# Optimization experiments

Hardware: AMD Instinct MI355X
Metric: run time of the kernel (lower is better)

Reference implementation:

```python
import jax, jax.numpy as jnp
import numpy as np

_DIMS = [15, 30, 60, 90, 120, 90, 60, 30, 15, 10, 5, 1]


def setup_inputs() -> dict:
    key = jax.random.key(0)
    keys = jax.random.split(key, 1 + 2 * 11)
    inp = {"x": jax.random.normal(keys[0], (524288, 15), dtype=jnp.float32)}
    for i in range(11):
        fan_in, fan_out = _DIMS[i], _DIMS[i + 1]
        bound = 1.0 / np.sqrt(fan_in)
        inp[f"W{i+1}"] = jax.random.uniform(keys[1 + 2 * i], (fan_out, fan_in), minval=-bound, maxval=bound, dtype=jnp.float32)
        inp[f"b{i+1}"] = jax.random.uniform(keys[2 + 2 * i], (fan_out,), minval=-bound, maxval=bound, dtype=jnp.float32)
    return inp


def reference(x, W1, b1, W2, b2, W3, b3, W4, b4, W5, b5, W6, b6, W7, b7, W8, b8, W9, b9, W10, b10, W11, b11):
    Ws = [W1, W2, W3, W4, W5, W6, W7, W8, W9, W10, W11]
    bs = [b1, b2, b3, b4, b5, b6, b7, b8, b9, b10, b11]
    h = x
    # 10 Linear+ReLU layers, funnel 15->30->60->90->120->90->60->30->15->10->5
    for W, b in zip(Ws[:-1], bs[:-1]):
        h = jax.nn.relu(h @ W.T + b)
    # final Linear 5->1 + sigmoid
    return jax.nn.sigmoid(h @ Ws[-1].T + bs[-1])
```

## Files before the change

### kernel.cpp

```cpp
#include <hip/hip_runtime.h>
#include <math.h>


using bf16x8 = __attribute__((ext_vector_type(8))) short;
using f32x4  = __attribute__((ext_vector_type(4))) float;
using u16x8  = __attribute__((ext_vector_type(8))) unsigned short;
using u32x2  = __attribute__((ext_vector_type(2))) unsigned;
typedef __bf16 bf16x2_t __attribute__((ext_vector_type(2)));

namespace {
constexpr int NL = 11;
constexpr int IN_[NL]   = {15, 30, 60, 90, 120, 90, 60, 30, 15, 10, 5};
constexpr int OUT_[NL]  = {30, 60, 90, 120, 90, 60, 30, 15, 10, 5, 1};
constexpr int KP_[NL]   = {32, 32, 64, 96, 128, 96, 64, 32, 32, 32, 32};
constexpr int NP_[NL]   = {32, 64, 96, 128, 96, 64, 32, 16, 16, 16, 16};
constexpr int WOFF_[NL] = {0, 1024, 3072, 9216, 21504, 33792, 39936, 41984, 42496, 43008, 43520};
constexpr int WTOT      = 44032;
constexpr int ACT_OFF   = WTOT;
constexpr int WAVES     = 16;
constexpr int THREADS   = WAVES * 64;
constexpr int ROWS_PER_WAVE  = 16;
constexpr int ROWS_PER_BLOCK = WAVES * ROWS_PER_WAVE;
constexpr int ARENA     = 2048;
constexpr int LDS_BYTES = (WTOT + WAVES * ARENA) * 2;
}

__device__ __forceinline__ unsigned short f2bf(float f) {
    unsigned u = __float_as_uint(f);
    u += 0x7fffu + ((u >> 16) & 1u);
    return (unsigned short)(u >> 16);
}

__device__ __forceinline__ unsigned pk2(float a, float b) {
#if __has_builtin(__builtin_amdgcn_cvt_pk_bf16_f32)
    return __builtin_bit_cast(unsigned, __builtin_amdgcn_cvt_pk_bf16_f32(a, b));
#else
    bf16x2_t c;
    c[0] = (__bf16)a;
    c[1] = (__bf16)b;
    return __builtin_bit_cast(unsigned, c);
#endif
}

template <int L>
__device__ __forceinline__ void stage_w(const float* __restrict__ W,
                                        const float* __restrict__ B,
                                        short* wlds, int tid) {
    constexpr int KP = KP_[L], NP = NP_[L], INl = IN_[L], OUTl = OUT_[L];
    constexpr int NKT = KP / 32;
    for (int idx = tid; idx < NP * KP; idx += THREADS) {
        const int f    = idx >> 9;
        const int t    = idx & 511;
        const int quad = t >> 7;
        const int colc = (t >> 3) & 15;
        const int j    = t & 7;
        const int mt   = f / NKT;
        const int kt   = f - mt * NKT;
        const int m    = mt * 16 + colc;
        const int k    = kt * 32 + quad * 8 + j;
        float v = 0.f;
        if (m < OUTl) {
            if (k < INl) v = W[m * INl + k];
            else if (k == INl) v = B[m];
            else if (k == INl + 1) {
                float hf = __builtin_bit_cast(float, (unsigned)f2bf(B[m]) << 16);
                v = B[m] - hf;
            }
        } else if (m == OUTl || m == OUTl + 1) {
            if (k == INl) v = 1.f;
        }
        wlds[WOFF_[L] + idx] = (short)f2bf(v);
    }
}

template <int L>
__device__ __forceinline__ void layer_fwd(const short* __restrict__ wlds,
                                          short* buf, int col, int quad) {
    constexpr int KP   = KP_[L];
    constexpr int NP   = NP_[L];
    constexpr int NKT  = KP / 32;
    constexpr int NMT  = NP / 16;
    constexpr int KPN  = KP_[L + 1];
    const short* wl = wlds + WOFF_[L];
    const int fo = quad * 128 + col * 8;

    f32x4 acc[NMT];
#pragma unroll
    for (int mt = 0; mt < NMT; ++mt)
        acc[mt] = f32x4{0.f, 0.f, 0.f, 0.f};

#pragma unroll
    for (int kt = 0; kt < NKT; ++kt) {
        bf16x8 b0 = *(const bf16x8*)(buf + kt * 512 + fo);
#pragma unroll
        for (int mt = 0; mt < NMT; ++mt) {
            bf16x8 af = *(const bf16x8*)(wl + (mt * NKT + kt) * 512 + fo);
            acc[mt] = __builtin_amdgcn_mfma_f32_16x16x32_bf16(af, b0, acc[mt], 0, 0, 0);
        }
    }
#pragma unroll
    for (int mt = 0; mt < NMT; ++mt) {
        const int wbase = (mt >> 1) * 512 + ((mt & 1) * 2 + (quad >> 1)) * 128 + col * 8 + (quad & 1) * 4;
        u32x2 o;
        o[0] = pk2(fmaxf(acc[mt][0], 0.f), fmaxf(acc[mt][1], 0.f));
        o[1] = pk2(fmaxf(acc[mt][2], 0.f), fmaxf(acc[mt][3], 0.f));
        *(u32x2*)(buf + wbase) = o;
    }
    if constexpr (NP < KPN) {
        if (quad < 2) {
            u16x8 z = {0, 0, 0, 0, 0, 0, 0, 0};
            if (quad == 0) z[0] = (unsigned short)0x3F80;
            *(u16x8*)(buf + (2 + quad) * 128 + col * 8) = z;
        }
    }
}

__device__ __forceinline__ void layer_one(bf16x8 af, short* buf, int col, int quad) {
    const int fo = quad * 128 + col * 8;
    bf16x8 b0 = *(const bf16x8*)(buf + fo);
    f32x4 a0 = f32x4{0.f, 0.f, 0.f, 0.f};
    a0 = __builtin_amdgcn_mfma_f32_16x16x32_bf16(af, b0, a0, 0, 0, 0);
    const int wbase = (quad >> 1) * 128 + col * 8 + (quad & 1) * 4;
    u32x2 o0;
    o0[0] = pk2(fmaxf(a0[0], 0.f), fmaxf(a0[1], 0.f));
    o0[1] = pk2(fmaxf(a0[2], 0.f), fmaxf(a0[3], 0.f));
    *(u32x2*)(buf + wbase) = o0;
    if (quad < 2) {
        u16x8 z = {0, 0, 0, 0, 0, 0, 0, 0};
        if (quad == 0) z[0] = (unsigned short)0x3F80;
        *(u16x8*)(buf + (2 + quad) * 128 + col * 8) = z;
    }
}

__device__ __forceinline__ float4 ld4(const float* p) {
    float4 t;
    __builtin_memcpy(&t, p, 16);
    return t;
}

__device__ __forceinline__ void fetch_x(const float* __restrict__ x, int row0,
                                        int col, int quad, float4& a0) {
    const float* r0 = x + (long)(row0 + col) * 15;
    if (quad < 3) {
        a0 = ld4(r0 + quad * 4);
    } else {
        float4 t0 = ld4(r0 + 11);
        a0 = make_float4(t0.y, t0.z, t0.w, 1.f);
    }
}

__device__ __forceinline__ void stage_x(short* buf, float4 a0, int col, int quad) {
    const int off = (quad >> 1) * 128 + col * 8 + (quad & 1) * 4;
    u32x2 o0;
    o0[0] = pk2(a0.x, a0.y); o0[1] = pk2(a0.z, a0.w);
    *(u32x2*)(buf + off) = o0;
    if (quad < 2) {
        u16x8 z = {0, 0, 0, 0, 0, 0, 0, 0};
        if (quad == 0) z[0] = (unsigned short)0x3F80;
        *(u16x8*)(buf + (2 + quad) * 128 + col * 8) = z;
    }
}

extern "C" __global__ void __launch_bounds__(THREADS, 4)
mlp_fused(const float* __restrict__ x,
          const float* __restrict__ W0,  const float* __restrict__ B0,
          const float* __restrict__ W1,  const float* __restrict__ B1,
          const float* __restrict__ W2,  const float* __restrict__ B2,
          const float* __restrict__ W3,  const float* __restrict__ B3,
          const float* __restrict__ W4,  const float* __restrict__ B4,
          const float* __restrict__ W5,  const float* __restrict__ B5,
          const float* __restrict__ W6,  const float* __restrict__ B6,
          const float* __restrict__ W7,  const float* __restrict__ B7,
          const float* __restrict__ W8,  const float* __restrict__ B8,
          const float* __restrict__ W9,  const float* __restrict__ B9,
          const float* __restrict__ W10, const float* __restrict__ B10,
          float* __restrict__ out, int nchunks) {
    extern __shared__ short smem[];
    short* wlds = smem;
    short* act  = smem + ACT_OFF;

    const int tid = threadIdx.x;

    stage_w<0>(W0, B0, wlds, tid);
    stage_w<1>(W1, B1, wlds, tid);
    stage_w<2>(W2, B2, wlds, tid);
    stage_w<3>(W3, B3, wlds, tid);
    stage_w<4>(W4, B4, wlds, tid);
    stage_w<5>(W5, B5, wlds, tid);
    stage_w<6>(W6, B6, wlds, tid);
    stage_w<7>(W7, B7, wlds, tid);
    stage_w<8>(W8, B8, wlds, tid);
    stage_w<9>(W9, B9, wlds, tid);
    stage_w<10>(W10, B10, wlds, tid);
    __syncthreads();

    const int wave = tid >> 6;
    const int lane = tid & 63;
    const int col  = lane & 15;
    const int quad = lane >> 4;
    short* buf = act + wave * ARENA;
    const int fo = quad * 128 + col * 8;

    const bf16x8 w7  = *(const bf16x8*)(wlds + WOFF_[7]  + fo);
    const bf16x8 w8  = *(const bf16x8*)(wlds + WOFF_[8]  + fo);
    const bf16x8 w9  = *(const bf16x8*)(wlds + WOFF_[9]  + fo);
    const bf16x8 w10 = *(const bf16x8*)(wlds + WOFF_[10] + fo);

    int chunk = blockIdx.x;
    float4 xa;
    if (chunk < nchunks)
        fetch_x(x, chunk * ROWS_PER_BLOCK + wave * ROWS_PER_WAVE, col, quad, xa);

    for (; chunk < nchunks; chunk += gridDim.x) {
        const int row0 = chunk * ROWS_PER_BLOCK + wave * ROWS_PER_WAVE;
        stage_x(buf, xa, col, quad);

        const int nxt = chunk + gridDim.x;
        if (nxt < nchunks)
            fetch_x(x, nxt * ROWS_PER_BLOCK + wave * ROWS_PER_WAVE, col, quad, xa);

        layer_fwd<0>(wlds, buf, col, quad);
        layer_fwd<1>(wlds, buf, col, quad);
        layer_fwd<2>(wlds, buf, col, quad);
        layer_fwd<3>(wlds, buf, col, quad);
        layer_fwd<4>(wlds, buf, col, quad);
        layer_fwd<5>(wlds, buf, col, quad);
        layer_fwd<6>(wlds, buf, col, quad);
        layer_one(w7, buf, col, quad);
        layer_one(w8, buf, col, quad);
        layer_one(w9, buf, col, quad);

        {
            bf16x8 b0 = *(const bf16x8*)(buf + fo);
            f32x4 a0 = f32x4{0.f, 0.f, 0.f, 0.f};
            a0 = __builtin_amdgcn_mfma_f32_16x16x32_bf16(w10, b0, a0, 0, 0, 0);
            if (quad == 0)
                out[row0 + col] = 1.f / (1.f + __expf(-a0[0]));
        }
    }
}

extern "C" void kernel_launch(void* const* d_in, const int* in_sizes, int n_in,
                              void* d_out, int out_size, void* d_ws, size_t ws_size,
                              hipStream_t stream) {
    (void)n_in; (void)d_ws; (void)ws_size; (void)out_size;
    const float* x = (const float*)d_in[0];
    const float* W[11];
    const float* B[11];
    for (int i = 0; i < 11; ++i) {
        W[i] = (const float*)d_in[1 + 2 * i];
        B[i] = (const float*)d_in[2 + 2 * i];
    }
    const int nrows   = in_sizes[0] / 15;
    const int nchunks = nrows / ROWS_PER_BLOCK;

    hipFuncSetAttribute((const void*)mlp_fused,
                        hipFuncAttributeMaxDynamicSharedMemorySize, LDS_BYTES);

    mlp_fused<<<dim3(256), dim3(THREADS), LDS_BYTES, stream>>>(
        x,
        W[0], B[0], W[1], B[1], W[2], B[2], W[3], B[3], W[4], B[4],
        W[5], B[5], W[6], B[6], W[7], B[7], W[8], B[8], W[9], B[9],
        W[10], B[10],
        (float*)d_out, nchunks);
}
```

Baseline: 182.9 us.

## Keep activations in registers using 32x32x16 MFMA and permlane32 swaps

Replaces the 16x16x32 MFMA chain, which staged every layer's activations through a per-wave LDS arena, with 32x32x16 MFMA tiles whose outputs are repacked into the next layer's B operand in registers via permlane32_swap. Each wave now handles 32 rows, and LDS holds only the weights. This removes the per-layer LDS write/read round trips and the fence-style dependencies they create. In exchange, register pressure rises (f32x16 accumulators plus two register activation buffers), the launch-bounds occupancy hint is dropped, and the small tail layers are padded to 32 outputs, which adds wasted MFMA work.

```diff
diff --git a/kernel.cpp b/kernel.cpp
--- a/kernel.cpp
+++ b/kernel.cpp
@@ -3,9 +3,9 @@
 
 
 using bf16x8 = __attribute__((ext_vector_type(8))) short;
-using f32x4  = __attribute__((ext_vector_type(4))) float;
-using u16x8  = __attribute__((ext_vector_type(8))) unsigned short;
-using u32x2  = __attribute__((ext_vector_type(2))) unsigned;
+using f32x16 = __attribute__((ext_vector_type(16))) float;
+using u32x2v = __attribute__((ext_vector_type(2))) unsigned;
+using u32x4  = __attribute__((ext_vector_type(4))) unsigned;
 typedef __bf16 bf16x2_t __attribute__((ext_vector_type(2)));
 
 namespace {
@@ -13,16 +13,15 @@
 constexpr int IN_[NL]   = {15, 30, 60, 90, 120, 90, 60, 30, 15, 10, 5};
 constexpr int OUT_[NL]  = {30, 60, 90, 120, 90, 60, 30, 15, 10, 5, 1};
 constexpr int KP_[NL]   = {32, 32, 64, 96, 128, 96, 64, 32, 32, 32, 32};
-constexpr int NP_[NL]   = {32, 64, 96, 128, 96, 64, 32, 16, 16, 16, 16};
-constexpr int WOFF_[NL] = {0, 1024, 3072, 9216, 21504, 33792, 39936, 41984, 42496, 43008, 43520};
-constexpr int WTOT      = 44032;
-constexpr int ACT_OFF   = WTOT;
+constexpr int NP_[NL]   = {32, 64, 96, 128, 96, 64, 32, 32, 32, 32, 32};
+constexpr int WOFF_[NL] = {0, 1024, 3072, 9216, 21504, 33792, 39936,
+                           41984, 43008, 44032, 45056};
+constexpr int WTOT      = 46080;
 constexpr int WAVES     = 16;
 constexpr int THREADS   = WAVES * 64;
-constexpr int ROWS_PER_WAVE  = 16;
+constexpr int ROWS_PER_WAVE  = 32;
 constexpr int ROWS_PER_BLOCK = WAVES * ROWS_PER_WAVE;
-constexpr int ARENA     = 2048;
-constexpr int LDS_BYTES = (WTOT + WAVES * ARENA) * 2;
+constexpr int LDS_BYTES = WTOT * 2;
 }
 
 __device__ __forceinline__ unsigned short f2bf(float f) {
@@ -42,22 +41,41 @@
 #endif
 }
 
+__device__ __forceinline__ u32x2v pls32(unsigned a, unsigned b) {
+#if __has_builtin(__builtin_amdgcn_permlane32_swap)
+    auto t = __builtin_amdgcn_permlane32_swap(a, b, false, false);
+    u32x2v r;
+    r[0] = t[0];
+    r[1] = t[1];
+    return r;
+#else
+    const int l = (int)(threadIdx.x & 63);
+    unsigned bl = (unsigned)__shfl((int)b, l & 31, 64);
+    unsigned ah = (unsigned)__shfl((int)a, l | 32, 64);
+    u32x2v r;
+    r[0] = (l < 32) ? a : bl;
+    r[1] = (l < 32) ? ah : b;
+    return r;
+#endif
+}
+
 template <int L>
 __device__ __forceinline__ void stage_w(const float* __restrict__ W,
                                         const float* __restrict__ B,
                                         short* wlds, int tid) {
     constexpr int KP = KP_[L], NP = NP_[L], INl = IN_[L], OUTl = OUT_[L];
-    constexpr int NKT = KP / 32;
+    constexpr int NKT = KP / 16;
     for (int idx = tid; idx < NP * KP; idx += THREADS) {
         const int f    = idx >> 9;
         const int t    = idx & 511;
-        const int quad = t >> 7;
-        const int colc = (t >> 3) & 15;
+        const int ln   = t >> 3;
         const int j    = t & 7;
+        const int mloc = ln & 31;
+        const int kh   = ln >> 5;
         const int mt   = f / NKT;
         const int kt   = f - mt * NKT;
-        const int m    = mt * 16 + colc;
-        const int k    = kt * 32 + quad * 8 + j;
+        const int m    = mt * 32 + mloc;
+        const int k    = kt * 16 + kh * 8 + j;
         float v = 0.f;
         if (m < OUTl) {
             if (k < INl) v = W[m * INl + k];
@@ -74,61 +92,32 @@
 }
 
 template <int L>
-__device__ __forceinline__ void layer_fwd(const short* __restrict__ wlds,
-                                          short* buf, int col, int quad) {
-    constexpr int KP   = KP_[L];
-    constexpr int NP   = NP_[L];
-    constexpr int NKT  = KP / 32;
-    constexpr int NMT  = NP / 16;
-    constexpr int KPN  = KP_[L + 1];
+__device__ __forceinline__ void layer(const short* __restrict__ wlds,
+                                      const u32x4* bin, u32x4* bout, int lofs) {
+    constexpr int NKT = KP_[L] / 16;
+    constexpr int NMT = NP_[L] / 32;
     const short* wl = wlds + WOFF_[L];
-    const int fo = quad * 128 + col * 8;
-
-    f32x4 acc[NMT];
-#pragma unroll
-    for (int mt = 0; mt < NMT; ++mt)
-        acc[mt] = f32x4{0.f, 0.f, 0.f, 0.f};
-
-#pragma unroll
-    for (int kt = 0; kt < NKT; ++kt) {
-        bf16x8 b0 = *(const bf16x8*)(buf + kt * 512 + fo);
-#pragma unroll
-        for (int mt = 0; mt < NMT; ++mt) {
-            bf16x8 af = *(const bf16x8*)(wl + (mt * NKT + kt) * 512 + fo);
-            acc[mt] = __builtin_amdgcn_mfma_f32_16x16x32_bf16(af, b0, acc[mt], 0, 0, 0);
+#pragma unroll
+    for (int mt = 0; mt < NMT; ++mt) {
+        f32x16 acc;
+#pragma unroll
+        for (int i = 0; i < 16; ++i) acc[i] = 0.f;
+#pragma unroll
+        for (int kt = 0; kt < NKT; ++kt) {
+            bf16x8 af = *(const bf16x8*)(wl + (mt * NKT + kt) * 512 + lofs);
+            acc = __builtin_amdgcn_mfma_f32_32x32x16_bf16(
+                af, __builtin_bit_cast(bf16x8, bin[kt]), acc, 0, 0, 0);
         }
-    }
-#pragma unroll
-    for (int mt = 0; mt < NMT; ++mt) {
-        const int wbase = (mt >> 1) * 512 + ((mt & 1) * 2 + (quad >> 1)) * 128 + col * 8 + (quad & 1) * 4;
-        u32x2 o;
-        o[0] = pk2(fmaxf(acc[mt][0], 0.f), fmaxf(acc[mt][1], 0.f));
-        o[1] = pk2(fmaxf(acc[mt][2], 0.f), fmaxf(acc[mt][3], 0.f));
-        *(u32x2*)(buf + wbase) = o;
-    }
-    if constexpr (NP < KPN) {
-        if (quad < 2) {
-            u16x8 z = {0, 0, 0, 0, 0, 0, 0, 0};
-            if (quad == 0) z[0] = (unsigned short)0x3F80;
-            *(u16x8*)(buf + (2 + quad) * 128 + col * 8) = z;
-        }
-    }
-}
-
-__device__ __forceinline__ void layer_one(bf16x8 af, short* buf, int col, int quad) {
-    const int fo = quad * 128 + col * 8;
-    bf16x8 b0 = *(const bf16x8*)(buf + fo);
-    f32x4 a0 = f32x4{0.f, 0.f, 0.f, 0.f};
-    a0 = __builtin_amdgcn_mfma_f32_16x16x32_bf16(af, b0, a0, 0, 0, 0);
-    const int wbase = (quad >> 1) * 128 + col * 8 + (quad & 1) * 4;
-    u32x2 o0;
-    o0[0] = pk2(fmaxf(a0[0], 0.f), fmaxf(a0[1], 0.f));
-    o0[1] = pk2(fmaxf(a0[2], 0.f), fmaxf(a0[3], 0.f));
-    *(u32x2*)(buf + wbase) = o0;
-    if (quad < 2) {
-        u16x8 z = {0, 0, 0, 0, 0, 0, 0, 0};
-        if (quad == 0) z[0] = (unsigned short)0x3F80;
-        *(u16x8*)(buf + (2 + quad) * 128 + col * 8) = z;
+        unsigned P[8];
+#pragma unroll
+        for (int i = 0; i < 8; ++i)
+            P[i] = pk2(fmaxf(acc[2 * i], 0.f), fmaxf(acc[2 * i + 1], 0.f));
+        u32x2v r02 = pls32(P[0], P[2]);
+        u32x2v r13 = pls32(P[1], P[3]);
+        u32x2v r46 = pls32(P[4], P[6]);
+        u32x2v r57 = pls32(P[5], P[7]);
+        bout[2 * mt]     = u32x4{r02[0], r13[0], r02[1], r13[1]};
+        bout[2 * mt + 1] = u32x4{r46[0], r57[0], r46[1], r57[1]};
     }
 }
 
@@ -138,30 +127,26 @@
     return t;
 }
 
-__device__ __forceinline__ void fetch_x(const float* __restrict__ x, int row0,
-                                        int col, int quad, float4& a0) {
-    const float* r0 = x + (long)(row0 + col) * 15;
-    if (quad < 3) {
-        a0 = ld4(r0 + quad * 4);
+__device__ __forceinline__ void fetch_x(const float* __restrict__ x, int row,
+                                        int h, float4& t0, float4& t1) {
+    const float* p = x + (long)row * 15;
+    if (h == 0) { t0 = ld4(p);     t1 = ld4(p + 4);  }
+    else        { t0 = ld4(p + 8); t1 = ld4(p + 11); }
+}
+
+__device__ __forceinline__ u32x4 pack_x(float4 t0, float4 t1, int h) {
+    u32x4 b;
+    if (h == 0) {
+        b[0] = pk2(t0.x, t0.y); b[1] = pk2(t0.z, t0.w);
+        b[2] = pk2(t1.x, t1.y); b[3] = pk2(t1.z, t1.w);
     } else {
-        float4 t0 = ld4(r0 + 11);
-        a0 = make_float4(t0.y, t0.z, t0.w, 1.f);
-    }
-}
-
-__device__ __forceinline__ void stage_x(short* buf, float4 a0, int col, int quad) {
-    const int off = (quad >> 1) * 128 + col * 8 + (quad & 1) * 4;
-    u32x2 o0;
-    o0[0] = pk2(a0.x, a0.y); o0[1] = pk2(a0.z, a0.w);
-    *(u32x2*)(buf + off) = o0;
-    if (quad < 2) {
-        u16x8 z = {0, 0, 0, 0, 0, 0, 0, 0};
-        if (quad == 0) z[0] = (unsigned short)0x3F80;
-        *(u16x8*)(buf + (2 + quad) * 128 + col * 8) = z;
-    }
-}
-
-extern "C" __global__ void __launch_bounds__(THREADS, 4)
+        b[0] = pk2(t0.x, t0.y); b[1] = pk2(t0.z, t0.w);
+        b[2] = pk2(t1.y, t1.z); b[3] = pk2(t1.w, 1.f);
+    }
+    return b;
+}
+
+extern "C" __global__ void __launch_bounds__(THREADS)
 mlp_fused(const float* __restrict__ x,
           const float* __restrict__ W0,  const float* __restrict__ B0,
           const float* __restrict__ W1,  const float* __restrict__ B1,
@@ -176,66 +161,66 @@
           const float* __restrict__ W10, const float* __restrict__ B10,
           float* __restrict__ out, int nchunks) {
     extern __shared__ short smem[];
-    short* wlds = smem;
-    short* act  = smem + ACT_OFF;
-
     const int tid = threadIdx.x;
 
-    stage_w<0>(W0, B0, wlds, tid);
-    stage_w<1>(W1, B1, wlds, tid);
-    stage_w<2>(W2, B2, wlds, tid);
-    stage_w<3>(W3, B3, wlds, tid);
-    stage_w<4>(W4, B4, wlds, tid);
-    stage_w<5>(W5, B5, wlds, tid);
-    stage_w<6>(W6, B6, wlds, tid);
-    stage_w<7>(W7, B7, wlds, tid);
-    stage_w<8>(W8, B8, wlds, tid);
-    stage_w<9>(W9, B9, wlds, tid);
-    stage_w<10>(W10, B10, wlds, tid);
+    stage_w<0>(W0, B0, smem, tid);
+    stage_w<1>(W1, B1, smem, tid);
+    stage_w<2>(W2, B2, smem, tid);
+    stage_w<3>(W3, B3, smem, tid);
+    stage_w<4>(W4, B4, smem, tid);
+    stage_w<5>(W5, B5, smem, tid);
+    stage_w<6>(W6, B6, smem, tid);
+    stage_w<7>(W7, B7, smem, tid);
+    stage_w<8>(W8, B8, smem, tid);
+    stage_w<9>(W9, B9, smem, tid);
+    stage_w<10>(W10, B10, smem, tid);
     __syncthreads();
 
     const int wave = tid >> 6;
     const int lane = tid & 63;
-    const int col  = lane & 15;
-    const int quad = lane >> 4;
-    short* buf = act + wave * ARENA;
-    const int fo = quad * 128 + col * 8;
-
-    const bf16x8 w7  = *(const bf16x8*)(wlds + WOFF_[7]  + fo);
-    const bf16x8 w8  = *(const bf16x8*)(wlds + WOFF_[8]  + fo);
-    const bf16x8 w9  = *(const bf16x8*)(wlds + WOFF_[9]  + fo);
-    const bf16x8 w10 = *(const bf16x8*)(wlds + WOFF_[10] + fo);
+    const int n    = lane & 31;
+    const int h    = lane >> 5;
+    const int lofs = lane * 8;
 
     int chunk = blockIdx.x;
-    float4 xa;
+    float4 t0, t1;
     if (chunk < nchunks)
-        fetch_x(x, chunk * ROWS_PER_BLOCK + wave * ROWS_PER_WAVE, col, quad, xa);
+        fetch_x(x, chunk * ROWS_PER_BLOCK + wave * ROWS_PER_WAVE + n, h, t0, t1);
 
     for (; chunk < nchunks; chunk += gridDim.x) {
         const int row0 = chunk * ROWS_PER_BLOCK + wave * ROWS_PER_WAVE;
-        stage_x(buf, xa, col, quad);
+
+        u32x4 bA[8], bB[6];
+        bA[0] = pack_x(t0, t1, h);
+        bA[1] = u32x4{h == 0 ? 0x3F80u : 0u, 0u, 0u, 0u};
 
         const int nxt = chunk + gridDim.x;
         if (nxt < nchunks)
-            fetch_x(x, nxt * ROWS_PER_BLOCK + wave * ROWS_PER_WAVE, col, quad, xa);
-
-        layer_fwd<0>(wlds, buf, col, quad);
-        layer_fwd<1>(wlds, buf, col, quad);
-        layer_fwd<2>(wlds, buf, col, quad);
-        layer_fwd<3>(wlds, buf, col, quad);
-        layer_fwd<4>(wlds, buf, col, quad);
-        layer_fwd<5>(wlds, buf, col, quad);
-        layer_fwd<6>(wlds, buf, col, quad);
-        layer_one(w7, buf, col, quad);
-        layer_one(w8, buf, col, quad);
-        layer_one(w9, buf, col, quad);
+            fetch_x(x, nxt * ROWS_PER_BLOCK + wave * ROWS_PER_WAVE + n, h, t0, t1);
+
+        layer<0>(smem, bA, bB, lofs);
+        layer<1>(smem, bB, bA, lofs);
+        layer<2>(smem, bA, bB, lofs);
+        layer<3>(smem, bB, bA, lofs);
+        layer<4>(smem, bA, bB, lofs);
+        layer<5>(smem, bB, bA, lofs);
+        layer<6>(smem, bA, bB, lofs);
+        layer<7>(smem, bB, bA, lofs);
+        layer<8>(smem, bA, bB, lofs);
+        layer<9>(smem, bB, bA, lofs);
 
         {
-            bf16x8 b0 = *(const bf16x8*)(buf + fo);
-            f32x4 a0 = f32x4{0.f, 0.f, 0.f, 0.f};
-            a0 = __builtin_amdgcn_mfma_f32_16x16x32_bf16(w10, b0, a0, 0, 0, 0);
-            if (quad == 0)
-                out[row0 + col] = 1.f / (1.f + __expf(-a0[0]));
+            f32x16 acc;
+#pragma unroll
+            for (int i = 0; i < 16; ++i) acc[i] = 0.f;
+#pragma unroll
+            for (int kt = 0; kt < 2; ++kt) {
+                bf16x8 af = *(const bf16x8*)(smem + WOFF_[10] + kt * 512 + lofs);
+                acc = __builtin_amdgcn_mfma_f32_32x32x16_bf16(
+                    af, __builtin_bit_cast(bf16x8, bA[kt]), acc, 0, 0, 0);
+            }
+            if (lane < 32)
+                out[row0 + lane] = 1.f / (1.f + __expf(-acc[0]));
         }
     }
 }
@@ -254,8 +239,8 @@
     const int nrows   = in_sizes[0] / 15;
     const int nchunks = nrows / ROWS_PER_BLOCK;
 
-    hipFuncSetAttribute((const void*)mlp_fused,
-                        hipFuncAttributeMaxDynamicSharedMemorySize, LDS_BYTES);
+    (void)hipFuncSetAttribute((const void*)mlp_fused,
+                              hipFuncAttributeMaxDynamicSharedMemorySize, LDS_BYTES);
 
     mlp_fused<<<dim3(256), dim3(THREADS), LDS_BYTES, stream>>>(
         x,
```

After: 481.6 us. +163.3%, slower.
